# Optimization experiments

Hardware: AMD Instinct MI355X
Metric: run time of the kernel (lower is better)

Reference implementation:

```python
import jax, jax.numpy as jnp
import numpy as np

B, D_IN, D_S = 16384, 1024, 1024


def setup_inputs() -> dict:
    key = jax.random.key(0)
    ks = jax.random.split(key, 7)
    s_in = 1.0 / np.sqrt(D_IN)
    s_h = 1.0 / np.sqrt(D_S)
    return {
        "input": jax.random.normal(ks[0], (B, D_IN), jnp.float32),
        "cell_state": jax.random.normal(ks[1], (B, D_S), jnp.float32),
        "hidden_state": jax.random.normal(ks[2], (B, D_S), jnp.float32),
        "Wx": jax.random.uniform(ks[3], (4, D_S, D_IN), jnp.float32, -s_in, s_in),
        "bx": jax.random.uniform(ks[4], (4, D_S), jnp.float32, -s_in, s_in),
        "Wh": jax.random.uniform(ks[5], (4, D_S, D_S), jnp.float32, -s_h, s_h),
        "bh": jax.random.uniform(ks[6], (4, D_S), jnp.float32, -s_h, s_h),
    }


def reference(input, cell_state, hidden_state, Wx, bx, Wh, bh):
    # Fused: two batched GEMMs produce all 4 gate pre-activations.
    # gates_x, gates_h: [4, B, D_S]; gate order: forget, input, cand, output
    gx = jnp.einsum('bi,gsi->gbs', input, Wx) + bx[:, None, :]
    gh = jnp.einsum('bh,gsh->gbs', hidden_state, Wh) + bh[:, None, :]
    pre = gx + gh
    f = jax.nn.sigmoid(pre[0])
    i = jax.nn.sigmoid(pre[1]) * jnp.tanh(pre[2])
    new_cell_state = cell_state * f + i
    output = jnp.tanh(new_cell_state) * jax.nn.sigmoid(pre[3])
    return (new_cell_state, output)
```

## Files before the change

kernel.cpp:

```cpp
#include <hip/hip_runtime.h>
#include <hip/hip_bf16.h>
#include <stdint.h>


typedef short bf16x8 __attribute__((ext_vector_type(8)));
typedef float f32x4 __attribute__((ext_vector_type(4)));

#define B_ROWS 16384
#define D_K 2048

__device__ __forceinline__ unsigned short f2bf(float f) {
    unsigned u = __builtin_bit_cast(unsigned, f);
    u += 0x7FFFu + ((u >> 16) & 1u);
    return (unsigned short)(u >> 16);
}

__device__ __forceinline__ float sigf(float x) { return 1.0f / (1.0f + __expf(-x)); }
__device__ __forceinline__ float tanhfast(float x) { return 2.0f / (1.0f + __expf(-2.0f * x)) - 1.0f; }

#define GLD16(gp, lp)                                                          \
    __builtin_amdgcn_global_load_lds(                                          \
        (const __attribute__((address_space(1))) unsigned int*)(gp),           \
        (__attribute__((address_space(3))) unsigned int*)(lp), 16, 0, 0)


__global__ void pack_A_kernel(const float* __restrict__ x,
                              const float* __restrict__ h,
                              unsigned short* __restrict__ A) {
    const int total = B_ROWS * (D_K / 4);
    for (int v = blockIdx.x * blockDim.x + threadIdx.x; v < total;
         v += gridDim.x * blockDim.x) {
        const int b = v >> 9;
        const int k0 = (v & 511) << 2;
        const float* src = (k0 < 1024) ? (x + (size_t)b * 1024 + k0)
                                       : (h + (size_t)b * 1024 + (k0 - 1024));
        float4 f = *(const float4*)src;
        unsigned p0 = (unsigned)f2bf(f.x) | ((unsigned)f2bf(f.y) << 16);
        unsigned p1 = (unsigned)f2bf(f.z) | ((unsigned)f2bf(f.w) << 16);
        uint2 o; o.x = p0; o.y = p1;
        *(uint2*)(A + (size_t)v * 4) = o;
    }
}

__global__ void pack_W_kernel(const float* __restrict__ Wx,
                              const float* __restrict__ Wh,
                              unsigned short* __restrict__ W) {
    const int total = 4096 * (D_K / 4);
    for (int v = blockIdx.x * blockDim.x + threadIdx.x; v < total;
         v += gridDim.x * blockDim.x) {
        const int n = v >> 9;
        const int k0 = (v & 511) << 2;
        const float* src = (k0 < 1024) ? (Wx + (size_t)n * 1024 + k0)
                                       : (Wh + (size_t)n * 1024 + (k0 - 1024));
        float4 f = *(const float4*)src;
        unsigned p0 = (unsigned)f2bf(f.x) | ((unsigned)f2bf(f.y) << 16);
        unsigned p1 = (unsigned)f2bf(f.z) | ((unsigned)f2bf(f.w) << 16);
        uint2 o; o.x = p0; o.y = p1;
        *(uint2*)(W + (size_t)v * 4) = o;
    }
}

__global__ void pack_bias_kernel(const float* __restrict__ bx,
                                 const float* __restrict__ bh,
                                 float* __restrict__ bias) {
    int i = blockIdx.x * blockDim.x + threadIdx.x;
    if (i < 4096) bias[i] = bx[i] + bh[i];
}


__global__ __launch_bounds__(512, 2) void lstm_gemm_kernel(
    const unsigned short* __restrict__ A,
    const unsigned short* __restrict__ W,
    const float* __restrict__ bias,
    const float* __restrict__ cell,
    float* __restrict__ out) {
    __shared__ __align__(16) unsigned short smem[24576];

    const int bid = blockIdx.x;
    const int wg = (bid & 7) * 256 + (bid >> 3);
    const int brow = (wg >> 4) << 7;
    const int bcol = (wg & 15) << 6;

    const int tid = threadIdx.x;
    const int wid = tid >> 6;
    const int lane = tid & 63;
    const int wr = wid >> 1, wc = wid & 1;
    const int lr = lane & 15, lg = lane >> 4;
    const int l8 = lane >> 3;
    const int lcol = (((lane & 7) ^ l8) << 3);

    f32x4 acc[4][2][2];
#pragma unroll
    for (int g = 0; g < 4; ++g)
#pragma unroll
        for (int m = 0; m < 2; ++m)
#pragma unroll
            for (int n = 0; n < 2; ++n) acc[g][m][n] = (f32x4){0.f, 0.f, 0.f, 0.f};

    const unsigned short* gp[6];
#pragma unroll
    for (int i = 0; i < 6; ++i) {
        const int c = wid * 6 + i;
        if (c < 16) {
            gp[i] = A + (size_t)(brow + c * 8 + l8) * D_K + lcol;
        } else {
            const int cw = c - 16;
            gp[i] = W + (size_t)((cw >> 3) * 1024 + bcol + (cw & 7) * 8 + l8) * D_K + lcol;
        }
    }

    for (int kt = 0; kt < D_K; kt += 64) {
#pragma unroll
        for (int i = 0; i < 6; ++i)
            GLD16(gp[i] + kt, (char*)smem + (wid * 6 + i) * 1024);
        asm volatile("s_waitcnt vmcnt(0)" ::: "memory");
        __syncthreads();

#pragma unroll
        for (int kk = 0; kk < 2; ++kk) {
            const int swk = (kk * 32 + lg * 8) ^ ((lr & 7) << 3);
            bf16x8 a[2];
#pragma unroll
            for (int m = 0; m < 2; ++m)
                a[m] = *(const bf16x8*)&smem[(wr * 32 + m * 16 + lr) * 64 + swk];
#pragma unroll
            for (int g = 0; g < 4; ++g) {
                const int wbase = 8192 + (g * 64 + wc * 32 + lr) * 64 + swk;
                bf16x8 w0 = *(const bf16x8*)&smem[wbase];
                bf16x8 w1 = *(const bf16x8*)&smem[wbase + 16 * 64];
#pragma unroll
                for (int m = 0; m < 2; ++m) {
                    acc[g][m][0] = __builtin_amdgcn_mfma_f32_16x16x32_bf16(a[m], w0, acc[g][m][0], 0, 0, 0);
                    acc[g][m][1] = __builtin_amdgcn_mfma_f32_16x16x32_bf16(a[m], w1, acc[g][m][1], 0, 0, 0);
                }
            }
        }
        __syncthreads();
    }

    float bv[4][2];
#pragma unroll
    for (int g = 0; g < 4; ++g)
#pragma unroll
        for (int n = 0; n < 2; ++n)
            bv[g][n] = bias[(g << 10) + bcol + wc * 32 + n * 16 + lr];

    float* outc = out;
    float* outh = out + (size_t)B_ROWS * 1024;
#pragma unroll
    for (int m = 0; m < 2; ++m) {
#pragma unroll
        for (int r = 0; r < 4; ++r) {
            const int b = brow + wr * 32 + m * 16 + lg * 4 + r;
            const size_t base = (size_t)b * 1024 + bcol + wc * 32;
#pragma unroll
            for (int n = 0; n < 2; ++n) {
                const int so = n * 16 + lr;
                float pf = acc[0][m][n][r] + bv[0][n];
                float pi = acc[1][m][n][r] + bv[1][n];
                float pc = acc[2][m][n][r] + bv[2][n];
                float po = acc[3][m][n][r] + bv[3][n];
                float cl = cell[base + so];
                float nc = cl * sigf(pf) + sigf(pi) * tanhfast(pc);
                outc[base + so] = nc;
                outh[base + so] = tanhfast(nc) * sigf(po);
            }
        }
    }
}


__global__ void lstm_naive_kernel(const float* __restrict__ x,
                                  const float* __restrict__ cell,
                                  const float* __restrict__ h,
                                  const float* __restrict__ Wx,
                                  const float* __restrict__ bx,
                                  const float* __restrict__ Wh,
                                  const float* __restrict__ bh,
                                  float* __restrict__ out) {
    int idx = blockIdx.x * blockDim.x + threadIdx.x;
    if (idx >= B_ROWS * 1024) return;
    int b = idx >> 10, s = idx & 1023;
    const float* xr = x + (size_t)b * 1024;
    const float* hr = h + (size_t)b * 1024;
    float pre[4];
#pragma unroll
    for (int g = 0; g < 4; ++g) {
        float acc = bx[(g << 10) + s] + bh[(g << 10) + s];
        const float* wx = Wx + ((size_t)(g << 10) + s) * 1024;
        const float* wh = Wh + ((size_t)(g << 10) + s) * 1024;
        for (int k = 0; k < 1024; ++k) acc += xr[k] * wx[k] + hr[k] * wh[k];
        pre[g] = acc;
    }
    float nc = cell[idx] * sigf(pre[0]) + sigf(pre[1]) * tanhfast(pre[2]);
    out[idx] = nc;
    out[(size_t)B_ROWS * 1024 + idx] = tanhfast(nc) * sigf(pre[3]);
}


extern "C" void kernel_launch(void* const* d_in, const int* in_sizes, int n_in,
                              void* d_out, int out_size, void* d_ws, size_t ws_size,
                              hipStream_t stream) {
    const float* x    = (const float*)d_in[0];
    const float* cell = (const float*)d_in[1];
    const float* hid  = (const float*)d_in[2];
    const float* Wx   = (const float*)d_in[3];
    const float* bx   = (const float*)d_in[4];
    const float* Wh   = (const float*)d_in[5];
    const float* bh   = (const float*)d_in[6];
    float* out = (float*)d_out;

    const size_t szA = (size_t)B_ROWS * D_K * 2;
    const size_t szW = (size_t)4096 * D_K * 2;
    const size_t szB = 4096 * 4;
    if (ws_size < szA + szW + szB) {
        lstm_naive_kernel<<<(B_ROWS * 1024) / 256, 256, 0, stream>>>(
            x, cell, hid, Wx, bx, Wh, bh, out);
        return;
    }

    unsigned short* Ab = (unsigned short*)d_ws;
    unsigned short* Wb = (unsigned short*)((char*)d_ws + szA);
    float* bias = (float*)((char*)d_ws + szA + szW);

    pack_A_kernel<<<8192, 256, 0, stream>>>(x, hid, Ab);
    pack_W_kernel<<<2048, 256, 0, stream>>>(Wx, Wh, Wb);
    pack_bias_kernel<<<16, 256, 0, stream>>>(bx, bh, bias);

    lstm_gemm_kernel<<<2048, 512, 0, stream>>>(Ab, Wb, bias, cell, out);
}
```

Before: 321.6 us.

## Double-buffer LDS staging and double the GEMM row tile to 256

The GEMM kernel now uses two LDS buffers, so global-to-LDS loads for the next K slice are issued before computing the current one, with a partial vmcnt wait in place of a full drain. The block row tile grows from 128 to 256 rows, which doubles the accumulators per wave and halves the grid to 1024 blocks, giving more reuse of each loaded weight tile. This costs 128KB of LDS per block and a larger accumulator register footprint. That likely limits occupancy to one block per CU even though the launch bounds still request two.

Measured after the change: 315.8 us. About the same (-1.8%).

```diff
diff --git a/kernel.cpp b/kernel.cpp
--- a/kernel.cpp
+++ b/kernel.cpp
@@ -74,11 +74,11 @@
     const float* __restrict__ bias,
     const float* __restrict__ cell,
     float* __restrict__ out) {
-    __shared__ __align__(16) unsigned short smem[24576];
+    __shared__ __align__(16) unsigned short smem[2][32768];
 
     const int bid = blockIdx.x;
-    const int wg = (bid & 7) * 256 + (bid >> 3);
-    const int brow = (wg >> 4) << 7;
+    const int wg = (bid & 7) * 128 + (bid >> 3);
+    const int brow = (wg >> 4) << 8;
     const int bcol = (wg & 15) << 6;
 
     const int tid = threadIdx.x;
@@ -89,54 +89,84 @@
     const int l8 = lane >> 3;
     const int lcol = (((lane & 7) ^ l8) << 3);
 
-    f32x4 acc[4][2][2];
+    f32x4 acc[4][4][2];
 #pragma unroll
     for (int g = 0; g < 4; ++g)
 #pragma unroll
-        for (int m = 0; m < 2; ++m)
+        for (int m = 0; m < 4; ++m)
 #pragma unroll
             for (int n = 0; n < 2; ++n) acc[g][m][n] = (f32x4){0.f, 0.f, 0.f, 0.f};
 
-    const unsigned short* gp[6];
-#pragma unroll
-    for (int i = 0; i < 6; ++i) {
-        const int c = wid * 6 + i;
-        if (c < 16) {
+    const unsigned short* gp[8];
+#pragma unroll
+    for (int i = 0; i < 8; ++i) {
+        const int c = wid * 8 + i;
+        if (c < 32) {
             gp[i] = A + (size_t)(brow + c * 8 + l8) * D_K + lcol;
         } else {
-            const int cw = c - 16;
+            const int cw = c - 32;
             gp[i] = W + (size_t)((cw >> 3) * 1024 + bcol + (cw & 7) * 8 + l8) * D_K + lcol;
         }
     }
 
-    for (int kt = 0; kt < D_K; kt += 64) {
-#pragma unroll
-        for (int i = 0; i < 6; ++i)
-            GLD16(gp[i] + kt, (char*)smem + (wid * 6 + i) * 1024);
-        asm volatile("s_waitcnt vmcnt(0)" ::: "memory");
-        __syncthreads();
-
-#pragma unroll
-        for (int kk = 0; kk < 2; ++kk) {
-            const int swk = (kk * 32 + lg * 8) ^ ((lr & 7) << 3);
-            bf16x8 a[2];
-#pragma unroll
-            for (int m = 0; m < 2; ++m)
-                a[m] = *(const bf16x8*)&smem[(wr * 32 + m * 16 + lr) * 64 + swk];
-#pragma unroll
-            for (int g = 0; g < 4; ++g) {
-                const int wbase = 8192 + (g * 64 + wc * 32 + lr) * 64 + swk;
-                bf16x8 w0 = *(const bf16x8*)&smem[wbase];
-                bf16x8 w1 = *(const bf16x8*)&smem[wbase + 16 * 64];
-#pragma unroll
-                for (int m = 0; m < 2; ++m) {
-                    acc[g][m][0] = __builtin_amdgcn_mfma_f32_16x16x32_bf16(a[m], w0, acc[g][m][0], 0, 0, 0);
-                    acc[g][m][1] = __builtin_amdgcn_mfma_f32_16x16x32_bf16(a[m], w1, acc[g][m][1], 0, 0, 0);
-                }
-            }
-        }
-        __syncthreads();
-    }
+    char* const lds0 = (char*)smem + (size_t)wid * 8 * 1024;
+
+#define STAGE(buf, kt)                                                         \
+    do {                                                                       \
+        char* _d = lds0 + (size_t)(buf) * 65536;                               \
+        _Pragma("unroll")                                                      \
+        for (int _i = 0; _i < 8; ++_i)                                         \
+            GLD16(gp[_i] + (kt), _d + _i * 1024);                              \
+    } while (0)
+
+#define COMPUTE(buf)                                                           \
+    do {                                                                       \
+        const unsigned short* _sA = smem[buf];                                 \
+        const unsigned short* _sW = smem[buf] + 16384;                         \
+        _Pragma("unroll")                                                      \
+        for (int kk = 0; kk < 2; ++kk) {                                       \
+            const int swk = (kk * 32 + lg * 8) ^ ((lr & 7) << 3);              \
+            bf16x8 a[4];                                                       \
+            _Pragma("unroll")                                                  \
+            for (int m = 0; m < 4; ++m)                                        \
+                a[m] = *(const bf16x8*)&_sA[(wr * 64 + m * 16 + lr) * 64 + swk]; \
+            _Pragma("unroll")                                                  \
+            for (int g = 0; g < 4; ++g) {                                      \
+                const int wbase = (g * 64 + wc * 32 + lr) * 64 + swk;          \
+                bf16x8 w0 = *(const bf16x8*)&_sW[wbase];                       \
+                bf16x8 w1 = *(const bf16x8*)&_sW[wbase + 16 * 64];             \
+                _Pragma("unroll")                                              \
+                for (int m = 0; m < 4; ++m) {                                  \
+                    acc[g][m][0] = __builtin_amdgcn_mfma_f32_16x16x32_bf16(    \
+                        a[m], w0, acc[g][m][0], 0, 0, 0);                      \
+                    acc[g][m][1] = __builtin_amdgcn_mfma_f32_16x16x32_bf16(    \
+                        a[m], w1, acc[g][m][1], 0, 0, 0);                      \
+                }                                                              \
+            }                                                                  \
+        }                                                                      \
+    } while (0)
+
+    STAGE(0, 0);
+
+    int cur = 0;
+    for (int t = 0; t < 31; ++t) {
+        STAGE(cur ^ 1, (t + 1) * 64);
+        asm volatile("s_waitcnt vmcnt(8)" ::: "memory");
+        __builtin_amdgcn_s_barrier();
+        asm volatile("" ::: "memory");
+        COMPUTE(cur);
+        asm volatile("" ::: "memory");
+        __builtin_amdgcn_s_barrier();
+        asm volatile("" ::: "memory");
+        cur ^= 1;
+    }
+    asm volatile("s_waitcnt vmcnt(0)" ::: "memory");
+    __builtin_amdgcn_s_barrier();
+    asm volatile("" ::: "memory");
+    COMPUTE(cur);
+
+#undef STAGE
+#undef COMPUTE
 
     float bv[4][2];
 #pragma unroll
@@ -148,10 +178,10 @@
     float* outc = out;
     float* outh = out + (size_t)B_ROWS * 1024;
 #pragma unroll
-    for (int m = 0; m < 2; ++m) {
+    for (int m = 0; m < 4; ++m) {
 #pragma unroll
         for (int r = 0; r < 4; ++r) {
-            const int b = brow + wr * 32 + m * 16 + lg * 4 + r;
+            const int b = brow + wr * 64 + m * 16 + lg * 4 + r;
             const size_t base = (size_t)b * 1024 + bcol + wc * 32;
 #pragma unroll
             for (int n = 0; n < 2; ++n) {
@@ -227,5 +257,5 @@
     pack_W_kernel<<<2048, 256, 0, stream>>>(Wx, Wh, Wb);
     pack_bias_kernel<<<16, 256, 0, stream>>>(bx, bh, bias);
 
-    lstm_gemm_kernel<<<2048, 512, 0, stream>>>(Ab, Wb, bias, cell, out);
-}
+    lstm_gemm_kernel<<<1024, 512, 0, stream>>>(Ab, Wb, bias, cell, out);
+}
```

## Double-buffer LDS with interleaved staged loads and larger 256-row GEMM tiles

Applied to the files above, without the earlier changes.

Restructures the fused LSTM GEMM to use double-buffered LDS where global-to-LDS loads for the next k-tile are issued in quarters between MFMA phases, with setprio around compute. The block tile grows to 256 rows with each wave computing 128x16 per gate, which raises fragment reuse and halves the grid. This targets the exposed load latency of the previous load-wait-compute loop. It costs more LDS (128KB, likely one block per CU) and more accumulator registers.

Result: slower. 337.4 us (+4.9%).

```diff
diff --git a/kernel.cpp b/kernel.cpp
--- a/kernel.cpp
+++ b/kernel.cpp
@@ -22,6 +22,10 @@
     __builtin_amdgcn_global_load_lds(                                          \
         (const __attribute__((address_space(1))) unsigned int*)(gp),           \
         (__attribute__((address_space(3))) unsigned int*)(lp), 16, 0, 0)
+
+#define FENCE() asm volatile("" ::: "memory")
+#define BARRIER()                                                              \
+    do { __builtin_amdgcn_s_barrier(); FENCE(); } while (0)
 
 
 __global__ void pack_A_kernel(const float* __restrict__ x,
@@ -74,97 +78,179 @@
     const float* __restrict__ bias,
     const float* __restrict__ cell,
     float* __restrict__ out) {
-    __shared__ __align__(16) unsigned short smem[24576];
+    __shared__ __align__(16) unsigned short smem[2][4][8192];
 
     const int bid = blockIdx.x;
-    const int wg = (bid & 7) * 256 + (bid >> 3);
-    const int brow = (wg >> 4) << 7;
-    const int bcol = (wg & 15) << 6;
+    const int wg = (bid & 7) * 128 + (bid >> 3);
+    const int brow = (wg & 63) << 8;
+    const int bcol = (wg >> 6) << 6;
 
     const int tid = threadIdx.x;
     const int wid = tid >> 6;
     const int lane = tid & 63;
-    const int wr = wid >> 1, wc = wid & 1;
+    const int wr = wid >> 2;
+    const int wc = wid & 3;
     const int lr = lane & 15, lg = lane >> 4;
     const int l8 = lane >> 3;
     const int lcol = (((lane & 7) ^ l8) << 3);
 
-    f32x4 acc[4][2][2];
+    f32x4 acc[4][8];
 #pragma unroll
     for (int g = 0; g < 4; ++g)
 #pragma unroll
-        for (int m = 0; m < 2; ++m)
-#pragma unroll
-            for (int n = 0; n < 2; ++n) acc[g][m][n] = (f32x4){0.f, 0.f, 0.f, 0.f};
-
-    const unsigned short* gp[6];
-#pragma unroll
-    for (int i = 0; i < 6; ++i) {
-        const int c = wid * 6 + i;
-        if (c < 16) {
-            gp[i] = A + (size_t)(brow + c * 8 + l8) * D_K + lcol;
-        } else {
-            const int cw = c - 16;
-            gp[i] = W + (size_t)((cw >> 3) * 1024 + bcol + (cw & 7) * 8 + l8) * D_K + lcol;
+        for (int m = 0; m < 8; ++m) acc[g][m] = (f32x4){0.f, 0.f, 0.f, 0.f};
+
+    const unsigned short* gpA[2][2];
+#pragma unroll
+    for (int ah = 0; ah < 2; ++ah)
+#pragma unroll
+        for (int i = 0; i < 2; ++i)
+            gpA[ah][i] = A + (size_t)(brow + ah * 128 + (2 * wid + i) * 8 + l8) * D_K + lcol;
+    const unsigned short* gpW[2][2];
+#pragma unroll
+    for (int wh = 0; wh < 2; ++wh)
+#pragma unroll
+        for (int i = 0; i < 2; ++i) {
+            const int rw = (2 * wid + i) * 8 + l8;
+            gpW[wh][i] = W + (size_t)((2 * wh + (rw >> 6)) * 1024 + bcol + (rw & 63)) * D_K + lcol;
         }
-    }
-
-    for (int kt = 0; kt < D_K; kt += 64) {
-#pragma unroll
-        for (int i = 0; i < 6; ++i)
-            GLD16(gp[i] + kt, (char*)smem + (wid * 6 + i) * 1024);
-        asm volatile("s_waitcnt vmcnt(0)" ::: "memory");
-        __syncthreads();
-
+
+#define STAGE_HALF(dbbase, half, gparr, kt)                                    \
+    do {                                                                       \
+        GLD16(gparr[0] + (kt), (dbbase) + (half) * 16384 + (2 * wid) * 1024);  \
+        GLD16(gparr[1] + (kt), (dbbase) + (half) * 16384 + (2 * wid + 1) * 1024); \
+    } while (0)
+
+    {
+        char* db = (char*)smem[0][0];
+        STAGE_HALF(db, 0, gpA[0], 0);
+        STAGE_HALF(db, 1, gpA[1], 0);
+        STAGE_HALF(db, 2, gpW[0], 0);
+        STAGE_HALF(db, 3, gpW[1], 0);
+        asm volatile("s_waitcnt vmcnt(2)" ::: "memory");
+        BARRIER();
+    }
+
+    const int swk0 = (lg * 8) ^ ((lr & 7) << 3);
+    const int swk1 = (32 + lg * 8) ^ ((lr & 7) << 3);
+
+    bf16x8 a[8], w[4];
+
+    for (int t = 0; t < 31; ++t) {
+        const unsigned short* sb = smem[t & 1][0];
+        char* db = (char*)smem[(t & 1) ^ 1][0];
+        const int kt2 = (t + 1) * 64;
+
+#pragma unroll
+        for (int m = 0; m < 8; ++m)
+            a[m] = *(const bf16x8*)&sb[wr * 8192 + (m * 16 + lr) * 64 + swk0];
+        w[0] = *(const bf16x8*)&sb[2 * 8192 + (wc * 16 + lr) * 64 + swk0];
+        w[1] = *(const bf16x8*)&sb[2 * 8192 + (64 + wc * 16 + lr) * 64 + swk0];
+        STAGE_HALF(db, 0, gpA[0], kt2);
+        asm volatile("s_waitcnt vmcnt(2)" ::: "memory");
+        BARRIER();
+        __builtin_amdgcn_s_setprio(1);
+#pragma unroll
+        for (int m = 0; m < 8; ++m)
+            acc[0][m] = __builtin_amdgcn_mfma_f32_16x16x32_bf16(a[m], w[0], acc[0][m], 0, 0, 0);
+#pragma unroll
+        for (int m = 0; m < 8; ++m)
+            acc[1][m] = __builtin_amdgcn_mfma_f32_16x16x32_bf16(a[m], w[1], acc[1][m], 0, 0, 0);
+        __builtin_amdgcn_s_setprio(0);
+        FENCE();
+        BARRIER();
+
+        w[2] = *(const bf16x8*)&sb[3 * 8192 + (wc * 16 + lr) * 64 + swk0];
+        w[3] = *(const bf16x8*)&sb[3 * 8192 + (64 + wc * 16 + lr) * 64 + swk0];
+        STAGE_HALF(db, 1, gpA[1], kt2);
+        BARRIER();
+        __builtin_amdgcn_s_setprio(1);
+#pragma unroll
+        for (int m = 0; m < 8; ++m)
+            acc[2][m] = __builtin_amdgcn_mfma_f32_16x16x32_bf16(a[m], w[2], acc[2][m], 0, 0, 0);
+#pragma unroll
+        for (int m = 0; m < 8; ++m)
+            acc[3][m] = __builtin_amdgcn_mfma_f32_16x16x32_bf16(a[m], w[3], acc[3][m], 0, 0, 0);
+        __builtin_amdgcn_s_setprio(0);
+        FENCE();
+        BARRIER();
+
+#pragma unroll
+        for (int m = 0; m < 8; ++m)
+            a[m] = *(const bf16x8*)&sb[wr * 8192 + (m * 16 + lr) * 64 + swk1];
+        w[0] = *(const bf16x8*)&sb[2 * 8192 + (wc * 16 + lr) * 64 + swk1];
+        w[1] = *(const bf16x8*)&sb[2 * 8192 + (64 + wc * 16 + lr) * 64 + swk1];
+        STAGE_HALF(db, 2, gpW[0], kt2);
+        BARRIER();
+        __builtin_amdgcn_s_setprio(1);
+#pragma unroll
+        for (int m = 0; m < 8; ++m)
+            acc[0][m] = __builtin_amdgcn_mfma_f32_16x16x32_bf16(a[m], w[0], acc[0][m], 0, 0, 0);
+#pragma unroll
+        for (int m = 0; m < 8; ++m)
+            acc[1][m] = __builtin_amdgcn_mfma_f32_16x16x32_bf16(a[m], w[1], acc[1][m], 0, 0, 0);
+        __builtin_amdgcn_s_setprio(0);
+        FENCE();
+        BARRIER();
+
+        w[2] = *(const bf16x8*)&sb[3 * 8192 + (wc * 16 + lr) * 64 + swk1];
+        w[3] = *(const bf16x8*)&sb[3 * 8192 + (64 + wc * 16 + lr) * 64 + swk1];
+        STAGE_HALF(db, 3, gpW[1], kt2);
+        asm volatile("s_waitcnt vmcnt(2)" ::: "memory");
+        BARRIER();
+        __builtin_amdgcn_s_setprio(1);
+#pragma unroll
+        for (int m = 0; m < 8; ++m)
+            acc[2][m] = __builtin_amdgcn_mfma_f32_16x16x32_bf16(a[m], w[2], acc[2][m], 0, 0, 0);
+#pragma unroll
+        for (int m = 0; m < 8; ++m)
+            acc[3][m] = __builtin_amdgcn_mfma_f32_16x16x32_bf16(a[m], w[3], acc[3][m], 0, 0, 0);
+        __builtin_amdgcn_s_setprio(0);
+        FENCE();
+        BARRIER();
+    }
+
+    asm volatile("s_waitcnt vmcnt(0)" ::: "memory");
+    BARRIER();
+    {
+        const unsigned short* sb = smem[1][0];
 #pragma unroll
         for (int kk = 0; kk < 2; ++kk) {
             const int swk = (kk * 32 + lg * 8) ^ ((lr & 7) << 3);
-            bf16x8 a[2];
-#pragma unroll
-            for (int m = 0; m < 2; ++m)
-                a[m] = *(const bf16x8*)&smem[(wr * 32 + m * 16 + lr) * 64 + swk];
+#pragma unroll
+            for (int m = 0; m < 8; ++m)
+                a[m] = *(const bf16x8*)&sb[wr * 8192 + (m * 16 + lr) * 64 + swk];
 #pragma unroll
             for (int g = 0; g < 4; ++g) {
-                const int wbase = 8192 + (g * 64 + wc * 32 + lr) * 64 + swk;
-                bf16x8 w0 = *(const bf16x8*)&smem[wbase];
-                bf16x8 w1 = *(const bf16x8*)&smem[wbase + 16 * 64];
-#pragma unroll
-                for (int m = 0; m < 2; ++m) {
-                    acc[g][m][0] = __builtin_amdgcn_mfma_f32_16x16x32_bf16(a[m], w0, acc[g][m][0], 0, 0, 0);
-                    acc[g][m][1] = __builtin_amdgcn_mfma_f32_16x16x32_bf16(a[m], w1, acc[g][m][1], 0, 0, 0);
-                }
+                const bf16x8 wv = *(const bf16x8*)&sb[(2 + (g >> 1)) * 8192 + ((g & 1) * 64 + wc * 16 + lr) * 64 + swk];
+#pragma unroll
+                for (int m = 0; m < 8; ++m)
+                    acc[g][m] = __builtin_amdgcn_mfma_f32_16x16x32_bf16(a[m], wv, acc[g][m], 0, 0, 0);
             }
         }
-        __syncthreads();
-    }
-
-    float bv[4][2];
-#pragma unroll
-    for (int g = 0; g < 4; ++g)
-#pragma unroll
-        for (int n = 0; n < 2; ++n)
-            bv[g][n] = bias[(g << 10) + bcol + wc * 32 + n * 16 + lr];
+    }
+#undef STAGE_HALF
+
+    float bv[4];
+#pragma unroll
+    for (int g = 0; g < 4; ++g) bv[g] = bias[(g << 10) + bcol + wc * 16 + lr];
 
     float* outc = out;
     float* outh = out + (size_t)B_ROWS * 1024;
 #pragma unroll
-    for (int m = 0; m < 2; ++m) {
+    for (int m = 0; m < 8; ++m) {
 #pragma unroll
         for (int r = 0; r < 4; ++r) {
-            const int b = brow + wr * 32 + m * 16 + lg * 4 + r;
-            const size_t base = (size_t)b * 1024 + bcol + wc * 32;
-#pragma unroll
-            for (int n = 0; n < 2; ++n) {
-                const int so = n * 16 + lr;
-                float pf = acc[0][m][n][r] + bv[0][n];
-                float pi = acc[1][m][n][r] + bv[1][n];
-                float pc = acc[2][m][n][r] + bv[2][n];
-                float po = acc[3][m][n][r] + bv[3][n];
-                float cl = cell[base + so];
-                float nc = cl * sigf(pf) + sigf(pi) * tanhfast(pc);
-                outc[base + so] = nc;
-                outh[base + so] = tanhfast(nc) * sigf(po);
-            }
+            const int b = brow + wr * 128 + m * 16 + lg * 4 + r;
+            const size_t idx = (size_t)b * 1024 + bcol + wc * 16 + lr;
+            float pf = acc[0][m][r] + bv[0];
+            float pi = acc[1][m][r] + bv[1];
+            float pc = acc[2][m][r] + bv[2];
+            float po = acc[3][m][r] + bv[3];
+            float cl = cell[idx];
+            float nc = cl * sigf(pf) + sigf(pi) * tanhfast(pc);
+            outc[idx] = nc;
+            outh[idx] = tanhfast(nc) * sigf(po);
         }
     }
 }
@@ -227,5 +313,5 @@
     pack_W_kernel<<<2048, 256, 0, stream>>>(Wx, Wh, Wb);
     pack_bias_kernel<<<16, 256, 0, stream>>>(bx, bh, bias);
 
-    lstm_gemm_kernel<<<2048, 512, 0, stream>>>(Ab, Wb, bias, cell, out);
-}
+    lstm_gemm_kernel<<<1024, 512, 0, stream>>>(Ab, Wb, bias, cell, out);
+}
```
